# Kernel optimization log

Hardware: AMD Instinct MI355X
Metric: run time of the kernel (lower is better)

## Reference

```python
import jax, jax.numpy as jnp
import numpy as np


def setup_inputs() -> dict:
    key = jax.random.key(0)
    k1, k2, k3 = jax.random.split(key, 3)
    B, C, H, Wd = 16, 768, 64, 64
    E = 16
    x = jax.random.normal(k1, (B, C, H, Wd), dtype=jnp.float32)
    # 1x1 conv weight [E, C] (Conv2d weight squeezed) and bias [E]
    W = jax.random.normal(k2, (E, C), dtype=jnp.float32) * (1.0 / np.sqrt(C))
    b = jax.random.normal(k3, (E,), dtype=jnp.float32) * 0.01
    return {"x": x, "W": W, "b": b, "active_experts": 2}


def reference(x, W, b, active_experts):
    # 1x1 conv == pointwise matmul over channel dim: [B,C,H,W] x [E,C] -> [B,E,H,W]
    logits = jnp.einsum("bchw,ec->behw", x, W) + b[None, :, None, None]
    scores = jax.nn.softmax(logits, axis=1)  # softmax over experts
    # top-k along expert axis: move E to last, take top-k, move back
    scores_last = jnp.moveaxis(scores, 1, -1)               # [B,H,W,E]
    topk_probs, topk_indices = jax.lax.top_k(scores_last, active_experts)  # [B,H,W,k]
    topk_probs = topk_probs / jnp.sum(topk_probs, axis=-1, keepdims=True)
    topk_probs = jnp.moveaxis(topk_probs, -1, 1)            # [B,k,H,W]
    topk_indices = jnp.moveaxis(topk_indices, -1, 1)        # [B,k,H,W]
    return topk_probs, topk_indices, scores
```

## Files before the change

### kernel.cpp

```cpp
#include <hip/hip_runtime.h>


#define C_DIM 768
#define E_DIM 16
#define HW    4096
#define NPIX  65536

__global__ __launch_bounds__(256) void transpose_w(
    const float* __restrict__ Wm, float* __restrict__ Wt)
{
    const int t = blockIdx.x * 256 + threadIdx.x;
    if (t < C_DIM * E_DIM) {
        const int e = t / C_DIM;
        const int c = t - e * C_DIM;
        Wt[c * E_DIM + e] = Wm[t];
    }
}

__global__ __launch_bounds__(256) void router_main(
    const float* __restrict__ x,
    const float* __restrict__ Wt,
    const float* __restrict__ bias,
    float* __restrict__ out)
{
    __shared__ float lds[4][128][17];

    const int logical = ((blockIdx.x & 7) << 6) + (blockIdx.x >> 3);

    const int p0  = logical * 128;
    const int b   = p0 >> 12;
    const int pb  = p0 & 4095;
    const int cg  = __builtin_amdgcn_readfirstlane(threadIdx.x >> 6);
    const int px2 = threadIdx.x & 63;
    const int c0  = cg * 192;

    const float* xp = x + (size_t)b * C_DIM * HW + pb + 2 * px2;

    float2 acc[E_DIM];
#pragma unroll
    for (int e = 0; e < E_DIM; ++e) acc[e] = make_float2(0.f, 0.f);

#pragma unroll 8
    for (int c = c0; c < c0 + 192; ++c) {
        const float2 xv = *reinterpret_cast<const float2*>(xp + (size_t)c * HW);
        const float4* wt = reinterpret_cast<const float4*>(Wt + c * E_DIM);
        const float4 w0 = wt[0], w1 = wt[1], w2 = wt[2], w3 = wt[3];
        acc[ 0].x = fmaf(xv.x, w0.x, acc[ 0].x); acc[ 0].y = fmaf(xv.y, w0.x, acc[ 0].y);
        acc[ 1].x = fmaf(xv.x, w0.y, acc[ 1].x); acc[ 1].y = fmaf(xv.y, w0.y, acc[ 1].y);
        acc[ 2].x = fmaf(xv.x, w0.z, acc[ 2].x); acc[ 2].y = fmaf(xv.y, w0.z, acc[ 2].y);
        acc[ 3].x = fmaf(xv.x, w0.w, acc[ 3].x); acc[ 3].y = fmaf(xv.y, w0.w, acc[ 3].y);
        acc[ 4].x = fmaf(xv.x, w1.x, acc[ 4].x); acc[ 4].y = fmaf(xv.y, w1.x, acc[ 4].y);
        acc[ 5].x = fmaf(xv.x, w1.y, acc[ 5].x); acc[ 5].y = fmaf(xv.y, w1.y, acc[ 5].y);
        acc[ 6].x = fmaf(xv.x, w1.z, acc[ 6].x); acc[ 6].y = fmaf(xv.y, w1.z, acc[ 6].y);
        acc[ 7].x = fmaf(xv.x, w1.w, acc[ 7].x); acc[ 7].y = fmaf(xv.y, w1.w, acc[ 7].y);
        acc[ 8].x = fmaf(xv.x, w2.x, acc[ 8].x); acc[ 8].y = fmaf(xv.y, w2.x, acc[ 8].y);
        acc[ 9].x = fmaf(xv.x, w2.y, acc[ 9].x); acc[ 9].y = fmaf(xv.y, w2.y, acc[ 9].y);
        acc[10].x = fmaf(xv.x, w2.z, acc[10].x); acc[10].y = fmaf(xv.y, w2.z, acc[10].y);
        acc[11].x = fmaf(xv.x, w2.w, acc[11].x); acc[11].y = fmaf(xv.y, w2.w, acc[11].y);
        acc[12].x = fmaf(xv.x, w3.x, acc[12].x); acc[12].y = fmaf(xv.y, w3.x, acc[12].y);
        acc[13].x = fmaf(xv.x, w3.y, acc[13].x); acc[13].y = fmaf(xv.y, w3.y, acc[13].y);
        acc[14].x = fmaf(xv.x, w3.z, acc[14].x); acc[14].y = fmaf(xv.y, w3.z, acc[14].y);
        acc[15].x = fmaf(xv.x, w3.w, acc[15].x); acc[15].y = fmaf(xv.y, w3.w, acc[15].y);
    }

#pragma unroll
    for (int e = 0; e < E_DIM; ++e) {
        lds[cg][2 * px2][e]     = acc[e].x;
        lds[cg][2 * px2 + 1][e] = acc[e].y;
    }
    __syncthreads();

    const int t = threadIdx.x;
    if (t < 128) {
        const int p = pb + t;

        float lg[E_DIM];
#pragma unroll
        for (int e = 0; e < E_DIM; ++e)
            lg[e] = bias[e] + lds[0][t][e] + lds[1][t][e] + lds[2][t][e] + lds[3][t][e];

        float m = -INFINITY;
#pragma unroll
        for (int e = 0; e < E_DIM; ++e) m = fmaxf(m, lg[e]);
        float pr[E_DIM];
        float sum = 0.0f;
#pragma unroll
        for (int e = 0; e < E_DIM; ++e) {
            pr[e] = __expf(lg[e] - m);
            sum += pr[e];
        }
        const float inv = 1.0f / sum;

        float* scores = out + 262144;
#pragma unroll
        for (int e = 0; e < E_DIM; ++e) {
            const float s = pr[e] * inv;
            pr[e] = s;
            scores[(size_t)(b * E_DIM + e) * HW + p] = s;
        }

        int i1 = 0;
        float p1 = pr[0];
#pragma unroll
        for (int e = 1; e < E_DIM; ++e)
            if (pr[e] > p1) { p1 = pr[e]; i1 = e; }
        int i2 = -1;
        float p2 = -INFINITY;
#pragma unroll
        for (int e = 0; e < E_DIM; ++e)
            if (e != i1 && pr[e] > p2) { p2 = pr[e]; i2 = e; }

        const float rs = 1.0f / (p1 + p2);
        const size_t o1 = (size_t)(b * 2 + 0) * HW + p;
        const size_t o2 = (size_t)(b * 2 + 1) * HW + p;
        out[o1] = p1 * rs;
        out[o2] = p2 * rs;
        float* idxo = out + 131072;
        idxo[o1] = (float)i1;
        idxo[o2] = (float)i2;
    }
}

__global__ __launch_bounds__(256) void topk_router_fused(
    const float* __restrict__ x, const float* __restrict__ Wm,
    const float* __restrict__ bias, float* __restrict__ out)
{
    const int g = blockIdx.x * 256 + threadIdx.x;
    const int b = g >> 12;
    const int p = g & 4095;
    const float* xp = x + (size_t)b * C_DIM * HW + p;

    float acc[E_DIM];
#pragma unroll
    for (int e = 0; e < E_DIM; ++e) acc[e] = 0.0f;
#pragma unroll 16
    for (int c = 0; c < C_DIM; ++c) {
        const float xv = xp[(size_t)c * HW];
#pragma unroll
        for (int e = 0; e < E_DIM; ++e)
            acc[e] = fmaf(xv, Wm[e * C_DIM + c], acc[e]);
    }
    float m = -INFINITY;
#pragma unroll
    for (int e = 0; e < E_DIM; ++e) { acc[e] += bias[e]; m = fmaxf(m, acc[e]); }
    float pr[E_DIM]; float sum = 0.0f;
#pragma unroll
    for (int e = 0; e < E_DIM; ++e) { pr[e] = __expf(acc[e] - m); sum += pr[e]; }
    const float inv = 1.0f / sum;
    float* scores = out + 262144;
#pragma unroll
    for (int e = 0; e < E_DIM; ++e) {
        const float s = pr[e] * inv; pr[e] = s;
        scores[(size_t)(b * E_DIM + e) * HW + p] = s;
    }
    int i1 = 0; float p1 = pr[0];
#pragma unroll
    for (int e = 1; e < E_DIM; ++e) if (pr[e] > p1) { p1 = pr[e]; i1 = e; }
    int i2 = -1; float p2 = -INFINITY;
#pragma unroll
    for (int e = 0; e < E_DIM; ++e) if (e != i1 && pr[e] > p2) { p2 = pr[e]; i2 = e; }
    const float rs = 1.0f / (p1 + p2);
    const size_t o1 = (size_t)(b * 2 + 0) * HW + p;
    const size_t o2 = (size_t)(b * 2 + 1) * HW + p;
    out[o1] = p1 * rs; out[o2] = p2 * rs;
    float* idxo = out + 131072;
    idxo[o1] = (float)i1; idxo[o2] = (float)i2;
}

extern "C" void kernel_launch(void* const* d_in, const int* in_sizes, int n_in,
                              void* d_out, int out_size, void* d_ws, size_t ws_size,
                              hipStream_t stream) {
    const float* x  = (const float*)d_in[0];
    const float* Wm = (const float*)d_in[1];
    const float* bs = (const float*)d_in[2];
    float* out = (float*)d_out;
    float* Wt  = (float*)d_ws;

    if (ws_size >= (size_t)C_DIM * E_DIM * sizeof(float)) {
        transpose_w<<<48, 256, 0, stream>>>(Wm, Wt);
        router_main<<<NPIX / 128, 256, 0, stream>>>(x, Wt, bs, out);
    } else {
        topk_router_fused<<<NPIX / 256, 256, 0, stream>>>(x, Wm, bs, out);
    }
}
```

Measured before the change: 40.71 us.

## Process four pixels per thread and reduce channel groups serially in LDS

Each thread now accumulates four pixels (float4 loads) instead of two, so each block covers 256 pixels and half as many blocks are launched. The cross-channel-group reduction now goes through a serial accumulate in a compact [E][256] LDS buffer, and all 256 threads run the softmax/top-k epilogue instead of 128. This cuts weight loads per FMA and doubles epilogue parallelism, but it doubles accumulator registers (64 floats), adds four barrier rounds, and leaves only 256 blocks, which may lower occupancy and latency hiding on a memory-bound kernel.

```diff
diff --git a/kernel.cpp b/kernel.cpp
--- a/kernel.cpp
+++ b/kernel.cpp
@@ -23,61 +23,89 @@
     const float* __restrict__ bias,
     float* __restrict__ out)
 {
-    __shared__ float lds[4][128][17];
-
-    const int logical = ((blockIdx.x & 7) << 6) + (blockIdx.x >> 3);
-
-    const int p0  = logical * 128;
+    __shared__ float red[E_DIM][256];
+
+    const int logical = ((blockIdx.x & 7) << 5) + (blockIdx.x >> 3);
+
+    const int p0  = logical * 256;
     const int b   = p0 >> 12;
     const int pb  = p0 & 4095;
     const int cg  = __builtin_amdgcn_readfirstlane(threadIdx.x >> 6);
-    const int px2 = threadIdx.x & 63;
+    const int ln  = threadIdx.x & 63;
     const int c0  = cg * 192;
 
-    const float* xp = x + (size_t)b * C_DIM * HW + pb + 2 * px2;
-
-    float2 acc[E_DIM];
-#pragma unroll
-    for (int e = 0; e < E_DIM; ++e) acc[e] = make_float2(0.f, 0.f);
+    const float* xp = x + (size_t)b * C_DIM * HW + pb + 4 * ln;
+
+    float4 acc[E_DIM];
+#pragma unroll
+    for (int e = 0; e < E_DIM; ++e) acc[e] = make_float4(0.f, 0.f, 0.f, 0.f);
 
 #pragma unroll 8
     for (int c = c0; c < c0 + 192; ++c) {
-        const float2 xv = *reinterpret_cast<const float2*>(xp + (size_t)c * HW);
+        const float4 xv = *reinterpret_cast<const float4*>(xp + (size_t)c * HW);
         const float4* wt = reinterpret_cast<const float4*>(Wt + c * E_DIM);
         const float4 w0 = wt[0], w1 = wt[1], w2 = wt[2], w3 = wt[3];
         acc[ 0].x = fmaf(xv.x, w0.x, acc[ 0].x); acc[ 0].y = fmaf(xv.y, w0.x, acc[ 0].y);
+        acc[ 0].z = fmaf(xv.z, w0.x, acc[ 0].z); acc[ 0].w = fmaf(xv.w, w0.x, acc[ 0].w);
         acc[ 1].x = fmaf(xv.x, w0.y, acc[ 1].x); acc[ 1].y = fmaf(xv.y, w0.y, acc[ 1].y);
+        acc[ 1].z = fmaf(xv.z, w0.y, acc[ 1].z); acc[ 1].w = fmaf(xv.w, w0.y, acc[ 1].w);
         acc[ 2].x = fmaf(xv.x, w0.z, acc[ 2].x); acc[ 2].y = fmaf(xv.y, w0.z, acc[ 2].y);
+        acc[ 2].z = fmaf(xv.z, w0.z, acc[ 2].z); acc[ 2].w = fmaf(xv.w, w0.z, acc[ 2].w);
         acc[ 3].x = fmaf(xv.x, w0.w, acc[ 3].x); acc[ 3].y = fmaf(xv.y, w0.w, acc[ 3].y);
+        acc[ 3].z = fmaf(xv.z, w0.w, acc[ 3].z); acc[ 3].w = fmaf(xv.w, w0.w, acc[ 3].w);
         acc[ 4].x = fmaf(xv.x, w1.x, acc[ 4].x); acc[ 4].y = fmaf(xv.y, w1.x, acc[ 4].y);
+        acc[ 4].z = fmaf(xv.z, w1.x, acc[ 4].z); acc[ 4].w = fmaf(xv.w, w1.x, acc[ 4].w);
         acc[ 5].x = fmaf(xv.x, w1.y, acc[ 5].x); acc[ 5].y = fmaf(xv.y, w1.y, acc[ 5].y);
+        acc[ 5].z = fmaf(xv.z, w1.y, acc[ 5].z); acc[ 5].w = fmaf(xv.w, w1.y, acc[ 5].w);
         acc[ 6].x = fmaf(xv.x, w1.z, acc[ 6].x); acc[ 6].y = fmaf(xv.y, w1.z, acc[ 6].y);
+        acc[ 6].z = fmaf(xv.z, w1.z, acc[ 6].z); acc[ 6].w = fmaf(xv.w, w1.z, acc[ 6].w);
         acc[ 7].x = fmaf(xv.x, w1.w, acc[ 7].x); acc[ 7].y = fmaf(xv.y, w1.w, acc[ 7].y);
+        acc[ 7].z = fmaf(xv.z, w1.w, acc[ 7].z); acc[ 7].w = fmaf(xv.w, w1.w, acc[ 7].w);
         acc[ 8].x = fmaf(xv.x, w2.x, acc[ 8].x); acc[ 8].y = fmaf(xv.y, w2.x, acc[ 8].y);
+        acc[ 8].z = fmaf(xv.z, w2.x, acc[ 8].z); acc[ 8].w = fmaf(xv.w, w2.x, acc[ 8].w);
         acc[ 9].x = fmaf(xv.x, w2.y, acc[ 9].x); acc[ 9].y = fmaf(xv.y, w2.y, acc[ 9].y);
+        acc[ 9].z = fmaf(xv.z, w2.y, acc[ 9].z); acc[ 9].w = fmaf(xv.w, w2.y, acc[ 9].w);
         acc[10].x = fmaf(xv.x, w2.z, acc[10].x); acc[10].y = fmaf(xv.y, w2.z, acc[10].y);
+        acc[10].z = fmaf(xv.z, w2.z, acc[10].z); acc[10].w = fmaf(xv.w, w2.z, acc[10].w);
         acc[11].x = fmaf(xv.x, w2.w, acc[11].x); acc[11].y = fmaf(xv.y, w2.w, acc[11].y);
+        acc[11].z = fmaf(xv.z, w2.w, acc[11].z); acc[11].w = fmaf(xv.w, w2.w, acc[11].w);
         acc[12].x = fmaf(xv.x, w3.x, acc[12].x); acc[12].y = fmaf(xv.y, w3.x, acc[12].y);
+        acc[12].z = fmaf(xv.z, w3.x, acc[12].z); acc[12].w = fmaf(xv.w, w3.x, acc[12].w);
         acc[13].x = fmaf(xv.x, w3.y, acc[13].x); acc[13].y = fmaf(xv.y, w3.y, acc[13].y);
+        acc[13].z = fmaf(xv.z, w3.y, acc[13].z); acc[13].w = fmaf(xv.w, w3.y, acc[13].w);
         acc[14].x = fmaf(xv.x, w3.z, acc[14].x); acc[14].y = fmaf(xv.y, w3.z, acc[14].y);
+        acc[14].z = fmaf(xv.z, w3.z, acc[14].z); acc[14].w = fmaf(xv.w, w3.z, acc[14].w);
         acc[15].x = fmaf(xv.x, w3.w, acc[15].x); acc[15].y = fmaf(xv.y, w3.w, acc[15].y);
-    }
-
-#pragma unroll
-    for (int e = 0; e < E_DIM; ++e) {
-        lds[cg][2 * px2][e]     = acc[e].x;
-        lds[cg][2 * px2 + 1][e] = acc[e].y;
-    }
+        acc[15].z = fmaf(xv.z, w3.w, acc[15].z); acc[15].w = fmaf(xv.w, w3.w, acc[15].w);
+    }
+
     __syncthreads();
-
-    const int t = threadIdx.x;
-    if (t < 128) {
+#pragma unroll
+    for (int s = 0; s < 4; ++s) {
+        if (cg == s) {
+            if (s == 0) {
+#pragma unroll
+                for (int e = 0; e < E_DIM; ++e)
+                    *reinterpret_cast<float4*>(&red[e][4 * ln]) = acc[e];
+            } else {
+#pragma unroll
+                for (int e = 0; e < E_DIM; ++e) {
+                    float4 r = *reinterpret_cast<float4*>(&red[e][4 * ln]);
+                    r.x += acc[e].x; r.y += acc[e].y; r.z += acc[e].z; r.w += acc[e].w;
+                    *reinterpret_cast<float4*>(&red[e][4 * ln]) = r;
+                }
+            }
+        }
+        __syncthreads();
+    }
+
+    {
+        const int t = threadIdx.x;
         const int p = pb + t;
 
         float lg[E_DIM];
 #pragma unroll
-        for (int e = 0; e < E_DIM; ++e)
-            lg[e] = bias[e] + lds[0][t][e] + lds[1][t][e] + lds[2][t][e] + lds[3][t][e];
+        for (int e = 0; e < E_DIM; ++e) lg[e] = bias[e] + red[e][t];
 
         float m = -INFINITY;
 #pragma unroll
@@ -178,7 +206,7 @@
 
     if (ws_size >= (size_t)C_DIM * E_DIM * sizeof(float)) {
         transpose_w<<<48, 256, 0, stream>>>(Wm, Wt);
-        router_main<<<NPIX / 128, 256, 0, stream>>>(x, Wt, bs, out);
+        router_main<<<NPIX / 256, 256, 0, stream>>>(x, Wt, bs, out);
     } else {
         topk_router_fused<<<NPIX / 256, 256, 0, stream>>>(x, Wm, bs, out);
     }
```

After: 88.88 us. +118.3%, slower.
